# Kernel tuning notes

Hardware: AMD Instinct MI355X
Metric: run time of the kernel (lower is better)

Reference implementation:

```python
import jax, jax.numpy as jnp
import numpy as np

NBINS = (128, 64, 32)
MIN_BIN_WIDTH = 1e-3
MIN_BIN_HEIGHT = 1e-3


def quadratic_spline(inputs, unnorm_widths, unnorm_heights):
    """Piecewise-quadratic CDF spline (nflows-style). inputs: (N,) in [0,1],
    unnorm_widths: (N, nb), unnorm_heights: (N, nb+1). Returns (outputs, logabsdet)."""
    num_bins = unnorm_widths.shape[-1]
    widths = jax.nn.softmax(unnorm_widths, axis=-1)
    widths = MIN_BIN_WIDTH + (1.0 - MIN_BIN_WIDTH * num_bins) * widths
    hexp = jnp.exp(unnorm_heights)
    # normalize piecewise-linear pdf to integrate to 1
    area = jnp.sum(0.5 * (hexp[:, :-1] + hexp[:, 1:]) * widths, axis=-1, keepdims=True)
    heights = hexp / area
    heights = MIN_BIN_HEIGHT + (1.0 - MIN_BIN_HEIGHT) * heights
    bin_cdf = jnp.cumsum(0.5 * (heights[:, :-1] + heights[:, 1:]) * widths, axis=-1)
    bin_left_cdf = jnp.pad(bin_cdf.at[:, -1].set(1.0), ((0, 0), (1, 0)))
    bin_loc = jnp.cumsum(widths, axis=-1)
    bin_locations = jnp.pad(bin_loc.at[:, -1].set(1.0), ((0, 0), (1, 0)))
    bin_idx = jnp.clip(jnp.sum((inputs[:, None] >= bin_locations).astype(jnp.int32), axis=-1) - 1,
                       0, num_bins - 1)[:, None]
    take = lambda t, i: jnp.take_along_axis(t, i, axis=-1)[:, 0]
    loc = take(bin_locations, bin_idx)
    w = take(widths, bin_idx)
    cdf = take(bin_left_cdf, bin_idx)
    hl = take(heights, bin_idx)
    hr = take(heights, bin_idx + 1)
    alpha = (inputs - loc) / w
    outputs = jnp.clip(0.5 * (hr - hl) * w * alpha * alpha + hl * w * alpha + cdf, 0.0, 1.0)
    logabsdet = jnp.log(alpha * (hr - hl) + hl)
    return outputs, logabsdet


def _forward(coordinates, clustering, delta_height_weight, delta_baseline_weight,
             unnormalized_heights, unnormalized_widths, baseline_bias,
             genes_oi, local_gene_ix, local_cellxgene_ix, localcellxgene_ix):
    n_total_genes = delta_baseline_weight.shape[0]
    # decoder
    dhw = delta_height_weight[genes_oi]                            # (G, L, K)
    mixture_delta = jnp.einsum('cl,glk->cgk', clustering, dhw)     # (C, G, K)
    baseline_delta = clustering @ delta_baseline_weight.T          # (C, n_total)
    baseline = jax.nn.softmax(jnp.log(baseline_bias)[None, :] + baseline_delta, axis=-1)
    baseline_cuts = baseline.reshape(-1)[localcellxgene_ix]        # (N,)
    delta = mixture_delta.reshape(-1, mixture_delta.shape[-1])[local_cellxgene_ix]  # (N, K)
    gene_global = genes_oi[local_gene_ix]                          # (N,)
    # quadratic spline stack log_prob (base = Uniform[0,1])
    x = coordinates
    logabsdet = jnp.zeros_like(coordinates)
    ho = 0
    wo = 0
    for n in NBINS:
        uh = unnormalized_heights[:, ho:ho + n][gene_global] + delta[:, ho:ho + n]
        uw = unnormalized_widths[:, wo:wo + n - 1][gene_global]
        x, lad = quadratic_spline(x, uw, uh)
        logabsdet = logabsdet + lad
        ho += n
        wo += n - 1
    likelihood_position = logabsdet
    likelihood_region = jnp.log(baseline_cuts) + jnp.log(jnp.asarray(n_total_genes, jnp.float32))
    elbo = -(likelihood_position + likelihood_region).sum()
    # KL regularization (scales = exp(log 1.0) = 1)
    half_log_2pi = float(0.5 * np.log(2.0 * np.pi))
    mixture_kl = -0.5 * dhw * dhw - half_log_2pi
    baseline_kl = -0.5 * jnp.square(delta_baseline_weight[genes_oi]) - half_log_2pi
    return elbo - mixture_kl.sum() - baseline_kl.sum()


def setup_inputs() -> dict:
    key = jax.random.key(0)
    ks = jax.random.split(key, 10)
    N, C, G, NT, L = 500_000, 1000, 500, 10_000, 16
    K = sum(NBINS)                # 224 heights / delta components
    W = sum(n - 1 for n in NBINS)  # 221 widths
    coordinates = jax.random.uniform(ks[0], (N,), jnp.float32, 1e-4, 1.0 - 1e-4)
    cluster_id = jax.random.randint(ks[1], (C,), 0, L)
    clustering = jax.nn.one_hot(cluster_id, L, dtype=jnp.float32)
    genes_oi = jnp.sort(jax.random.permutation(ks[2], NT)[:G]).astype(jnp.int32)
    cell_ix = jax.random.randint(ks[3], (N,), 0, C)
    local_gene_ix = jax.random.randint(ks[4], (N,), 0, G).astype(jnp.int32)
    local_cellxgene_ix = (cell_ix * G + local_gene_ix).astype(jnp.int32)
    localcellxgene_ix = (cell_ix * NT + genes_oi[local_gene_ix]).astype(jnp.int32)
    delta_height_weight = jax.random.normal(ks[5], (NT, L, K), jnp.float32) * 0.05
    delta_baseline_weight = jax.random.uniform(ks[6], (NT, L), jnp.float32, -0.25, 0.25)
    unnormalized_heights = jax.random.normal(ks[7], (NT, K), jnp.float32) * 0.1
    unnormalized_widths = jax.random.normal(ks[8], (NT, W), jnp.float32) * 0.1
    baseline_bias = jax.random.uniform(ks[9], (NT,), jnp.float32, 1e-5, 1.0)
    return {
        'coordinates': coordinates, 'clustering': clustering,
        'delta_height_weight': delta_height_weight,
        'delta_baseline_weight': delta_baseline_weight,
        'unnormalized_heights': unnormalized_heights,
        'unnormalized_widths': unnormalized_widths,
        'baseline_bias': baseline_bias,
        'genes_oi': genes_oi, 'local_gene_ix': local_gene_ix,
        'local_cellxgene_ix': local_cellxgene_ix,
        'localcellxgene_ix': localcellxgene_ix,
    }


def reference(coordinates, clustering, delta_height_weight, delta_baseline_weight,
              unnormalized_heights, unnormalized_widths, baseline_bias,
              genes_oi, local_gene_ix, local_cellxgene_ix, localcellxgene_ix):
    return _forward(coordinates, clustering, delta_height_weight, delta_baseline_weight,
                    unnormalized_heights, unnormalized_widths, baseline_bias,
                    genes_oi, local_gene_ix, local_cellxgene_ix, localcellxgene_ix)
```

## Files before the change

### kernel.cpp

```cpp
#include <hip/hip_runtime.h>
#include <math.h>


#define CAP 192
static constexpr float  F_MBW = 1e-3f;
static constexpr float  F_MBH = 1e-3f;
static constexpr double D_HL2PI = 0.918938533204672741780329736406;


__global__ void __launch_bounds__(256)
kA(const float* __restrict__ clustering, int* __restrict__ cid,
   double* __restrict__ dpart, int* __restrict__ cnt, int C, int L, int P) {
  int bid = blockIdx.x, tid = threadIdx.x;
  if (bid < 4) {
    int c = bid * 256 + tid;
    if (c < C) {
      const float* row = clustering + (size_t)c * L;
      int best = 0; float bv = row[0];
      for (int l = 1; l < L; ++l) { float v = row[l]; if (v > bv) { bv = v; best = l; } }
      cid[c] = best;
    }
  } else {
    if (bid == 4 && tid < 128) dpart[tid] = 0.0;
    int i = (bid - 4) * 256 + tid;
    if (i < P) cnt[i] = 0;
  }
}

__global__ void __launch_bounds__(256)
kB(const float* __restrict__ coords, const int* __restrict__ lgi,
   const int* __restrict__ lcg, const int* __restrict__ cid,
   const float* __restrict__ bb, const float* __restrict__ dbw,
   int* __restrict__ cnt, float* __restrict__ xs, double* __restrict__ dpart,
   int N, int G, int L, int NT, int SCAT) {
  int bid = blockIdx.x;
  if (bid < SCAT) {
    int n0 = (bid * 256 + threadIdx.x) * 2;
    #pragma unroll
    for (int q = 0; q < 2; ++q) {
      int n = n0 + q;
      if (n < N) {
        int pair = lgi[n] * L + cid[lcg[n] / G];
        int pos = atomicAdd(&cnt[pair], 1);
        if (pos < CAP) xs[(size_t)pair * CAP + pos] = coords[n];
      }
    }
  } else {
    int g = (bid - SCAT) * 256 + threadIdx.x;
    float s[16];
    #pragma unroll
    for (int l = 0; l < 16; ++l) s[l] = 0.f;
    if (g < NT) {
      float b = bb[g];
      const float4* row = (const float4*)(dbw + (size_t)g * 16);
      #pragma unroll
      for (int q = 0; q < 4; ++q) {
        float4 v = row[q];
        s[4 * q + 0] = b * expf(v.x); s[4 * q + 1] = b * expf(v.y);
        s[4 * q + 2] = b * expf(v.z); s[4 * q + 3] = b * expf(v.w);
      }
    }
    __shared__ float partl[4][16];
    int lane = threadIdx.x & 63, wv = threadIdx.x >> 6;
    #pragma unroll
    for (int l = 0; l < 16; ++l) {
      float v = s[l];
      for (int off = 32; off; off >>= 1) v += __shfl_xor(v, off);
      if (lane == 0) partl[wv][l] = v;
    }
    __syncthreads();
    if (threadIdx.x < 16) {
      float t = partl[0][threadIdx.x] + partl[1][threadIdx.x]
              + partl[2][threadIdx.x] + partl[3][threadIdx.x];
      atomicAdd(&dpart[threadIdx.x * 8], (double)t);
    }
  }
}

static __device__ __forceinline__ float wscan(float v, int lane) {
  #pragma unroll
  for (int off = 1; off < 64; off <<= 1) {
    float u = __shfl_up(v, off, 64);
    if (lane >= off) v += u;
  }
  return v;
}

__global__ void __launch_bounds__(64)
k_pair(const float* __restrict__ uh, const float* __restrict__ uw,
       const float* __restrict__ dhw, const int* __restrict__ genes_oi,
       const float* __restrict__ xs, const int* __restrict__ cnt,
       const float* __restrict__ bb, const float* __restrict__ dbw,
       const double* __restrict__ dpart,
       float* __restrict__ partA, float* __restrict__ partB,
       int L, int K, int W, int NT) {
  int p = blockIdx.x;
  int g = p / L;
  int cl = p - g * L;
  int gg = genes_oi[g];
  const float* uhg  = uh + (size_t)gg * K;
  const float* uwg  = uw + (size_t)gg * W;
  const float* drow = dhw + ((size_t)gg * L + cl) * K;
  int t = threadIdx.x;

  __shared__ float s_loc[224];
  __shared__ float s_cdf[224];
  __shared__ float s_hh[224];
  __shared__ int   grd[224];
  __shared__ float s_stg[128];

  const float cw128 = 1.0f - F_MBW * 127.0f;
  const float chh   = 1.0f - F_MBH;
  float d2;

  {
    int i0 = 2 * t, i1 = 2 * t + 1;
    float2 dv = *(const float2*)(drow + i0);
    float2 uv = *(const float2*)(uhg + i0);
    d2 = dv.x * dv.x + dv.y * dv.y;
    float hexp0 = expf(uv.x + dv.x), hexp1 = expf(uv.y + dv.y);
    s_stg[i0] = hexp0; s_stg[i1] = hexp1;
    float ew0 = expf(uwg[i0]);
    float ew1 = (i1 < 127) ? expf(uwg[i1]) : 0.f;
    float ps = wscan(ew0 + ew1, t);
    float wsum = __shfl(ps, 63);
    float incl0 = ps - ew1;
    float excl0 = incl0 - ew0, excl1 = incl0;
    float rw = cw128 / wsum;
    float width0 = F_MBW + rw * ew0;
    float width1 = F_MBW + rw * ew1;
    float loc0 = F_MBW * (float)i0 + rw * excl0;
    float loc1 = F_MBW * (float)i1 + rw * excl1;
    __syncthreads();
    float hn = (i1 < 127) ? s_stg[i1 + 1] : 0.f;
    float at0 = 0.5f * (hexp0 + hexp1) * width0;
    float at1 = (i1 < 127) ? 0.5f * (hexp1 + hn) * width1 : 0.f;
    float pa = wscan(at0 + at1, t);
    float area = __shfl(pa, 63);
    float aincl0 = pa - at1;
    float aexcl0 = aincl0 - at0, aexcl1 = aincl0;
    float ra = chh / area;
    float h0 = F_MBH + ra * hexp0, h1 = F_MBH + ra * hexp1;
    float cdf0 = F_MBH * loc0 + ra * aexcl0;
    float cdf1 = F_MBH * loc1 + ra * aexcl1;
    if (i1 == 127) { loc1 = 1.0f; cdf1 = 1.0f; }
    s_loc[i0] = loc0; s_cdf[i0] = cdf0; s_hh[i0] = h0;
    s_loc[i1] = loc1; s_cdf[i1] = cdf1; s_hh[i1] = h1;
  }

  int ho = 128, wo = 127, tb = 128;
  #pragma unroll
  for (int lev = 1; lev < 3; ++lev) {
    const int nbp1 = (lev == 1) ? 64 : 32;
    const int nb = nbp1 - 1;
    const float cwl = 1.0f - F_MBW * (float)nb;
    float dvx = (t < nbp1) ? drow[ho + t] : 0.f;
    d2 += dvx * dvx;
    float hexp = (t < nbp1) ? expf(uhg[ho + t] + dvx) : 0.f;
    __syncthreads();
    s_stg[t] = hexp;
    float ew = (t < nb) ? expf(uwg[wo + t]) : 0.f;
    float ips = wscan(ew, t);
    float wsum = __shfl(ips, nb - 1);
    float excl = ips - ew;
    float rw = cwl / wsum;
    float width = F_MBW + rw * ew;
    float loc = F_MBW * (float)t + rw * excl;
    __syncthreads();
    float hn = (t + 1 < nbp1) ? s_stg[t + 1] : 0.f;
    float at = (t < nb) ? 0.5f * (hexp + hn) * width : 0.f;
    float ipa = wscan(at, t);
    float area = __shfl(ipa, nb - 1);
    float aexcl = ipa - at;
    float ra = chh / area;
    float h = F_MBH + ra * hexp;
    float cdf = F_MBH * loc + ra * aexcl;
    if (t == nb) { loc = 1.0f; cdf = 1.0f; }
    if (t < nbp1) { s_loc[tb + t] = loc; s_cdf[tb + t] = cdf; s_hh[tb + t] = h; }
    ho += nbp1; wo += nb; tb += nbp1;
  }
  __syncthreads();

  {
    #pragma unroll
    for (int q = 0; q < 2; ++q) {
      int j = 2 * t + q;
      float target = (float)j * (1.0f / 128.0f);
      int lo = 0, hi = 128;
      #pragma unroll
      for (int it = 0; it < 7; ++it) {
        int mid = (lo + hi) >> 1;
        if (s_loc[mid] <= target) lo = mid; else hi = mid;
      }
      grd[j] = (lo > 126) ? 126 : lo;
    }
    {
      float target = (float)t * (1.0f / 64.0f);
      int lo = 0, hi = 64;
      #pragma unroll
      for (int it = 0; it < 6; ++it) {
        int mid = (lo + hi) >> 1;
        if (s_loc[128 + mid] <= target) lo = mid; else hi = mid;
      }
      grd[128 + t] = (lo > 62) ? 62 : lo;
    }
    if (t < 32) {
      float target = (float)t * (1.0f / 32.0f);
      int lo = 0, hi = 32;
      #pragma unroll
      for (int it = 0; it < 5; ++it) {
        int mid = (lo + hi) >> 1;
        if (s_loc[192 + mid] <= target) lo = mid; else hi = mid;
      }
      grd[192 + t] = (lo > 30) ? 30 : lo;
    }
  }
  __syncthreads();

  int m = cnt[p]; if (m > CAP) m = CAP;
  float lad_sum = 0.f;
  for (int i = t; i < m; i += 64) {
    float x = xs[(size_t)p * CAP + i];
    float lad = 0.f;
    int b2 = 0;
    #pragma unroll
    for (int lev = 0; lev < 3; ++lev) {
      const int nbp1 = (lev == 0) ? 128 : (lev == 1) ? 64 : 32;
      int j = (int)(x * (float)nbp1);
      j = (j > nbp1 - 1) ? (nbp1 - 1) : j;
      int idx = grd[b2 + j];
      while (idx > 0 && s_loc[b2 + idx] > x) --idx;
      while (idx < nbp1 - 2 && s_loc[b2 + idx + 1] <= x) ++idx;
      float la = s_loc[b2 + idx];
      float w  = s_loc[b2 + idx + 1] - la;
      float cd = s_cdf[b2 + idx];
      float hl = s_hh[b2 + idx];
      float hr = s_hh[b2 + idx + 1];
      float alpha = (x - la) / w;
      float dh = hr - hl;
      float outv = (0.5f * dh * alpha + hl) * (w * alpha) + cd;
      x = fminf(fmaxf(outv, 0.f), 1.f);
      lad += logf(alpha * dh + hl);
      b2 += nbp1;
    }
    lad_sum += lad;
  }
  #pragma unroll
  for (int off = 32; off; off >>= 1) {
    lad_sum += __shfl_xor(lad_sum, off);
    d2      += __shfl_xor(d2, off);
  }
  if (t == 0) {
    float dv = dbw[(size_t)gg * L + cl];
    float rc = logf(bb[gg]) + dv - logf((float)dpart[cl * 8]) + logf((float)NT);
    partA[p] = lad_sum + (float)m * rc;
    partB[p] = d2 + dv * dv;
  }
}

__global__ void __launch_bounds__(256)
k_final(const float* __restrict__ partA, const float* __restrict__ partB,
        float* __restrict__ out, int P, long long M12) {
  int tid = threadIdx.x;
  double sa = 0.0, sb = 0.0;
  for (int i = tid; i < P; i += 256) { sa += (double)partA[i]; sb += (double)partB[i]; }
  __shared__ double rA[256], rB[256];
  rA[tid] = sa; rB[tid] = sb;
  __syncthreads();
  for (int off = 128; off > 0; off >>= 1) {
    if (tid < off) { rA[tid] += rA[tid + off]; rB[tid] += rB[tid + off]; }
    __syncthreads();
  }
  if (tid == 0)
    out[0] = (float)(-rA[0] + 0.5 * rB[0] + (double)M12 * D_HL2PI);
}

extern "C" void kernel_launch(void* const* d_in, const int* in_sizes, int n_in,
                              void* d_out, int out_size, void* d_ws, size_t ws_size,
                              hipStream_t stream) {
  const float* coords     = (const float*)d_in[0];
  const float* clustering = (const float*)d_in[1];
  const float* dhw        = (const float*)d_in[2];
  const float* dbw        = (const float*)d_in[3];
  const float* uh         = (const float*)d_in[4];
  const float* uw         = (const float*)d_in[5];
  const float* bb         = (const float*)d_in[6];
  const int*   genes_oi   = (const int*)d_in[7];
  const int*   lgi        = (const int*)d_in[8];
  const int*   lcg        = (const int*)d_in[9];

  int N  = in_sizes[0];
  int NT = in_sizes[6];
  int L  = in_sizes[3] / NT;
  int C  = in_sizes[1] / L;
  int K  = in_sizes[4] / NT;
  int W  = in_sizes[5] / NT;
  int G  = in_sizes[7];
  int P  = G * L;

  char* ws = (char*)d_ws;
  double* dpart = (double*)ws;
  int*    cid   = (int*)(ws + 4096);
  int*    cnt   = (int*)(ws + 8192);
  float*  partA = (float*)(ws + 40960);
  float*  partB = (float*)(ws + 73728);
  float*  xs    = (float*)(ws + 131072);

  int SCAT = (N + 511) / 512;
  int LSEB = (NT + 255) / 256;

  hipLaunchKernelGGL(kA, dim3(4 + (P + 255) / 256), dim3(256), 0, stream,
                     clustering, cid, dpart, cnt, C, L, P);
  hipLaunchKernelGGL(kB, dim3(SCAT + LSEB), dim3(256), 0, stream,
                     coords, lgi, lcg, cid, bb, dbw, cnt, xs, dpart,
                     N, G, L, NT, SCAT);
  hipLaunchKernelGGL(k_pair, dim3(P), dim3(64), 0, stream,
                     uh, uw, dhw, genes_oi, xs, cnt, bb, dbw, dpart,
                     partA, partB, L, K, W, NT);
  hipLaunchKernelGGL(k_final, dim3(1), dim3(256), 0, stream,
                     partA, partB, (float*)d_out, P,
                     (long long)G * L * K + (long long)G * L);
}
```

Baseline: 59.20 us.

## Fuse width and area scans algebraically, coalesce scatter, widen final reduction

Area and CDF prefix sums are rewritten as linear combinations of prefix sums over exp-widths, averaged heights, and their products, so all three are computed in one combined warp scan. This removes the second dependent scan, the shared staging array and the barriers in each spline level. Neighbouring heights now come from a shuffle instead of shared memory. The scatter loop switches to a coalesced index pattern, and the final reduction block grows from 256 to 1024 threads. The rearranged sums may round slightly differently in float.

After: 55.41 us. 1.07x faster.

```diff
diff --git a/kernel.cpp b/kernel.cpp
--- a/kernel.cpp
+++ b/kernel.cpp
@@ -35,10 +35,10 @@
    int N, int G, int L, int NT, int SCAT) {
   int bid = blockIdx.x;
   if (bid < SCAT) {
-    int n0 = (bid * 256 + threadIdx.x) * 2;
+    int base = bid * 512;
     #pragma unroll
     for (int q = 0; q < 2; ++q) {
-      int n = n0 + q;
+      int n = base + q * 256 + threadIdx.x;
       if (n < N) {
         int pair = lgi[n] * L + cid[lcg[n] / G];
         int pos = atomicAdd(&cnt[pair], 1);
@@ -77,13 +77,14 @@
   }
 }
 
-static __device__ __forceinline__ float wscan(float v, int lane) {
+static __device__ __forceinline__ void wscan3(float& x, float& y, float& z, int lane) {
   #pragma unroll
   for (int off = 1; off < 64; off <<= 1) {
-    float u = __shfl_up(v, off, 64);
-    if (lane >= off) v += u;
-  }
-  return v;
+    float a = __shfl_up(x, off, 64);
+    float b = __shfl_up(y, off, 64);
+    float c = __shfl_up(z, off, 64);
+    if (lane >= off) { x += a; y += b; z += c; }
+  }
 }
 
 __global__ void __launch_bounds__(64)
@@ -107,45 +108,41 @@
   __shared__ float s_cdf[224];
   __shared__ float s_hh[224];
   __shared__ int   grd[224];
-  __shared__ float s_stg[128];
-
-  const float cw128 = 1.0f - F_MBW * 127.0f;
-  const float chh   = 1.0f - F_MBH;
+
+  const float chh = 1.0f - F_MBH;
   float d2;
 
   {
+    const float cw128 = 1.0f - F_MBW * 127.0f;
     int i0 = 2 * t, i1 = 2 * t + 1;
     float2 dv = *(const float2*)(drow + i0);
     float2 uv = *(const float2*)(uhg + i0);
     d2 = dv.x * dv.x + dv.y * dv.y;
-    float hexp0 = expf(uv.x + dv.x), hexp1 = expf(uv.y + dv.y);
-    s_stg[i0] = hexp0; s_stg[i1] = hexp1;
+    float h0 = expf(uv.x + dv.x), h1 = expf(uv.y + dv.y);
+    float h2 = __shfl_down(h0, 1, 64);
     float ew0 = expf(uwg[i0]);
     float ew1 = (i1 < 127) ? expf(uwg[i1]) : 0.f;
-    float ps = wscan(ew0 + ew1, t);
-    float wsum = __shfl(ps, 63);
-    float incl0 = ps - ew1;
-    float excl0 = incl0 - ew0, excl1 = incl0;
+    float a0 = 0.5f * (h0 + h1);
+    float a1 = (i1 < 127) ? 0.5f * (h1 + h2) : 0.f;
+    float b0 = a0 * ew0, b1 = a1 * ew1;
+    float sew = ew0 + ew1, sa = a0 + a1, sb = b0 + b1;
+    wscan3(sew, sa, sb, t);
+    float wsum = __shfl(sew, 63);
+    float S1   = __shfl(sa, 63);
+    float S2   = __shfl(sb, 63);
     float rw = cw128 / wsum;
-    float width0 = F_MBW + rw * ew0;
-    float width1 = F_MBW + rw * ew1;
-    float loc0 = F_MBW * (float)i0 + rw * excl0;
-    float loc1 = F_MBW * (float)i1 + rw * excl1;
-    __syncthreads();
-    float hn = (i1 < 127) ? s_stg[i1 + 1] : 0.f;
-    float at0 = 0.5f * (hexp0 + hexp1) * width0;
-    float at1 = (i1 < 127) ? 0.5f * (hexp1 + hn) * width1 : 0.f;
-    float pa = wscan(at0 + at1, t);
-    float area = __shfl(pa, 63);
-    float aincl0 = pa - at1;
-    float aexcl0 = aincl0 - at0, aexcl1 = aincl0;
+    float area = F_MBW * S1 + rw * S2;
     float ra = chh / area;
-    float h0 = F_MBH + ra * hexp0, h1 = F_MBH + ra * hexp1;
-    float cdf0 = F_MBH * loc0 + ra * aexcl0;
-    float cdf1 = F_MBH * loc1 + ra * aexcl1;
+    float E0 = sew - (ew0 + ew1), E1 = E0 + ew0;
+    float A0 = sa - (a0 + a1),    A1 = A0 + a0;
+    float B0 = sb - (b0 + b1),    B1 = B0 + b0;
+    float loc0 = F_MBW * (float)i0 + rw * E0;
+    float loc1 = F_MBW * (float)i1 + rw * E1;
+    float cdf0 = F_MBH * loc0 + ra * (F_MBW * A0 + rw * B0);
+    float cdf1 = F_MBH * loc1 + ra * (F_MBW * A1 + rw * B1);
     if (i1 == 127) { loc1 = 1.0f; cdf1 = 1.0f; }
-    s_loc[i0] = loc0; s_cdf[i0] = cdf0; s_hh[i0] = h0;
-    s_loc[i1] = loc1; s_cdf[i1] = cdf1; s_hh[i1] = h1;
+    s_loc[i0] = loc0; s_cdf[i0] = cdf0; s_hh[i0] = F_MBH + ra * h0;
+    s_loc[i1] = loc1; s_cdf[i1] = cdf1; s_hh[i1] = F_MBH + ra * h1;
   }
 
   int ho = 128, wo = 127, tb = 128;
@@ -157,24 +154,22 @@
     float dvx = (t < nbp1) ? drow[ho + t] : 0.f;
     d2 += dvx * dvx;
     float hexp = (t < nbp1) ? expf(uhg[ho + t] + dvx) : 0.f;
-    __syncthreads();
-    s_stg[t] = hexp;
+    float hn = __shfl_down(hexp, 1, 64);
     float ew = (t < nb) ? expf(uwg[wo + t]) : 0.f;
-    float ips = wscan(ew, t);
-    float wsum = __shfl(ips, nb - 1);
-    float excl = ips - ew;
+    float a  = (t < nb) ? 0.5f * (hexp + hn) : 0.f;
+    float b  = a * ew;
+    float sew = ew, sa = a, sb = b;
+    wscan3(sew, sa, sb, t);
+    float wsum = __shfl(sew, 63);
+    float S1   = __shfl(sa, 63);
+    float S2   = __shfl(sb, 63);
     float rw = cwl / wsum;
-    float width = F_MBW + rw * ew;
-    float loc = F_MBW * (float)t + rw * excl;
-    __syncthreads();
-    float hn = (t + 1 < nbp1) ? s_stg[t + 1] : 0.f;
-    float at = (t < nb) ? 0.5f * (hexp + hn) * width : 0.f;
-    float ipa = wscan(at, t);
-    float area = __shfl(ipa, nb - 1);
-    float aexcl = ipa - at;
+    float area = F_MBW * S1 + rw * S2;
     float ra = chh / area;
+    float E = sew - ew, A = sa - a, B = sb - b;
+    float loc = F_MBW * (float)t + rw * E;
+    float cdf = F_MBH * loc + ra * (F_MBW * A + rw * B);
     float h = F_MBH + ra * hexp;
-    float cdf = F_MBH * loc + ra * aexcl;
     if (t == nb) { loc = 1.0f; cdf = 1.0f; }
     if (t < nbp1) { s_loc[tb + t] = loc; s_cdf[tb + t] = cdf; s_hh[tb + t] = h; }
     ho += nbp1; wo += nb; tb += nbp1;
@@ -258,16 +253,16 @@
   }
 }
 
-__global__ void __launch_bounds__(256)
+__global__ void __launch_bounds__(1024)
 k_final(const float* __restrict__ partA, const float* __restrict__ partB,
         float* __restrict__ out, int P, long long M12) {
   int tid = threadIdx.x;
   double sa = 0.0, sb = 0.0;
-  for (int i = tid; i < P; i += 256) { sa += (double)partA[i]; sb += (double)partB[i]; }
-  __shared__ double rA[256], rB[256];
+  for (int i = tid; i < P; i += 1024) { sa += (double)partA[i]; sb += (double)partB[i]; }
+  __shared__ double rA[1024], rB[1024];
   rA[tid] = sa; rB[tid] = sb;
   __syncthreads();
-  for (int off = 128; off > 0; off >>= 1) {
+  for (int off = 512; off > 0; off >>= 1) {
     if (tid < off) { rA[tid] += rA[tid + off]; rB[tid] += rB[tid + off]; }
     __syncthreads();
   }
@@ -317,7 +312,7 @@
   hipLaunchKernelGGL(k_pair, dim3(P), dim3(64), 0, stream,
                      uh, uw, dhw, genes_oi, xs, cnt, bb, dbw, dpart,
                      partA, partB, L, K, W, NT);
-  hipLaunchKernelGGL(k_final, dim3(1), dim3(256), 0, stream,
+  hipLaunchKernelGGL(k_final, dim3(1), dim3(1024), 0, stream,
                      partA, partB, (float*)d_out, P,
                      (long long)G * L * K + (long long)G * L);
 }
```
